# Kernel tuning notes

Hardware: AMD Instinct MI355X
Metric: run time of the kernel (lower is better)

The kernel has to match this reference:

```python
import jax, jax.numpy as jnp
import numpy as np

E, H = 1024, 16
HD = E // H
QLEN, KLEN, BS = 1024, 2048, 4
PREV = KLEN - QLEN


def _rel_shift(x):
    # x: (q, k, b, h) -> Transformer-XL relative shift
    q, k, b, h = x.shape
    x = jnp.pad(x, ((0, 0), (1, 0), (0, 0), (0, 0)))  # (q, k+1, b, h)
    x = x.reshape(k + 1, q, b, h)[1:].reshape(q, k, b, h)
    return x


def setup_inputs() -> dict:
    key = jax.random.key(0)
    ks = jax.random.split(key, 16)
    s = 0.02  # weight init scale
    inp = {
        "query": jax.random.normal(ks[0], (QLEN, BS, E), jnp.float32),
        "key": jax.random.normal(ks[1], (KLEN, BS, E), jnp.float32),
        "value": jax.random.normal(ks[2], (KLEN, BS, E), jnp.float32),
        "pos_embedding": jax.random.normal(ks[3], (KLEN, 1, E), jnp.float32),
        "U": jax.random.normal(ks[4], (H, HD), jnp.float32) * s,
        "V": jax.random.normal(ks[5], (H, HD), jnp.float32) * s,
        "Wq": jax.random.normal(ks[6], (E, E), jnp.float32) * s,
        "bq": jnp.zeros((E,), jnp.float32),
        "Wk": jax.random.normal(ks[7], (E, E), jnp.float32) * s,
        "bk": jnp.zeros((E,), jnp.float32),
        "Wv": jax.random.normal(ks[8], (E, E), jnp.float32) * s,
        "bv": jnp.zeros((E,), jnp.float32),
        "Wp": jax.random.normal(ks[9], (E, E), jnp.float32) * s,
        "Wo": jax.random.normal(ks[10], (E, E), jnp.float32) * s,
        "bo": jnp.zeros((E,), jnp.float32),
    }
    # causal XL mask: query i attends to keys j <= i + PREV; True = masked
    qi = jnp.arange(QLEN)[:, None]
    kj = jnp.arange(KLEN)[None, :]
    inp["mask"] = (kj > qi + PREV)[:, :, None]  # (q, k, 1) bool
    return inp


def reference(query, key, value, pos_embedding, U, V, Wq, bq, Wk, bk, Wv, bv, Wp, Wo, bo, mask):
    q_len, b, e = query.shape
    k_len = key.shape[0]
    scale = float(np.sqrt(e))  # note: sqrt(embed_dim), as in the source

    queries = (query @ Wq + bq).reshape(q_len, b, H, HD)
    keys = (key @ Wk + bk).reshape(k_len, b, H, HD)
    values = (value @ Wv + bv).reshape(k_len, b, H, HD)
    R = (pos_embedding @ Wp).reshape(-1, H, HD)  # (k, H, HD)

    content_score = jnp.einsum('qbhd,kbhd->qkbh', queries + U, keys)
    position_score = jnp.einsum('qbhd,khd->qkbh', queries + V, R)
    position_score = _rel_shift(position_score)

    attention_score = (content_score + position_score) / scale
    attention_score = jnp.where(mask[..., None], jnp.float32(-1e20), attention_score)
    attention = jax.nn.softmax(attention_score, axis=1)

    alpha = jnp.einsum('qkbh,kbhd->qbhd', attention, values).reshape(q_len, b, e)
    return alpha @ Wo + bo
```

## Files before the change

kernel.cpp:

```cpp
#include <hip/hip_runtime.h>
#include <stdint.h>

#define QLEN 1024
#define KLEN 2048
#define BSZ  4
#define NH   16
#define HD   64
#define EMB  1024
#define PREVL 1024
#define SLOG2E 0.045084220027780106f

typedef __attribute__((ext_vector_type(4))) float f32x4;
typedef __attribute__((ext_vector_type(8))) short bf16x8;

__device__ __forceinline__ unsigned short f2bf(float f){
  unsigned u = __float_as_uint(f);
  u += 0x7fffu + ((u >> 16) & 1u);
  return (unsigned short)(u >> 16);
}

__device__ __forceinline__ void gload_lds16(const void* g, void* l){
  __builtin_amdgcn_global_load_lds((const __attribute__((address_space(1))) void*)g,
                                   (__attribute__((address_space(3))) void*)l, 16, 0, 0);
}

__global__ void txl_prep(const float* __restrict__ w0, const float* __restrict__ w1,
                         const float* __restrict__ w2, const float* __restrict__ w3,
                         const float* __restrict__ w4,
                         unsigned short* __restrict__ o0, unsigned short* __restrict__ o1,
                         unsigned short* __restrict__ o2, unsigned short* __restrict__ o3,
                         unsigned short* __restrict__ o4,
                         const float* __restrict__ q, const float* __restrict__ k,
                         const float* __restrict__ v, const float* __restrict__ p,
                         unsigned short* __restrict__ qo, unsigned short* __restrict__ ko,
                         unsigned short* __restrict__ vo, unsigned short* __restrict__ po){
  const int bid = blockIdx.x;
  if (bid < 5120){
    const int z = bid >> 10, rem = bid & 1023;
    const int by = rem >> 5, bx = rem & 31;
    const float* in; unsigned short* out;
    switch (z){
      case 0: in = w0; out = o0; break;
      case 1: in = w1; out = o1; break;
      case 2: in = w2; out = o2; break;
      case 3: in = w3; out = o3; break;
      default: in = w4; out = o4; break;
    }
    __shared__ float tile[32][33];
    int tx = threadIdx.x & 31, ty = threadIdx.x >> 5;
    int k0 = by * 32, n0 = bx * 32;
    #pragma unroll
    for (int j = 0; j < 32; j += 8)
      tile[ty + j][tx] = in[(size_t)(k0 + ty + j) * EMB + n0 + tx];
    __syncthreads();
    #pragma unroll
    for (int j = 0; j < 32; j += 8)
      out[(size_t)(n0 + ty + j) * EMB + k0 + tx] = f2bf(tile[tx][ty + j]);
  } else {
    for (size_t c = (size_t)(bid - 5120) * 256 + threadIdx.x; c < 2883584; c += (size_t)2048 * 256){
      const float* src; unsigned short* dst; size_t off;
      if (c < 524288)      { src = q; dst = qo; off = c; }
      else if (c < 1572864){ src = k; dst = ko; off = c - 524288; }
      else if (c < 2621440){ src = v; dst = vo; off = c - 1572864; }
      else                 { src = p; dst = po; off = c - 2621440; }
      f32x4 a = *(const f32x4*)(src + off * 8);
      f32x4 b = *(const f32x4*)(src + off * 8 + 4);
      bf16x8 r;
      #pragma unroll
      for (int u = 0; u < 4; ++u){ r[u] = (short)f2bf(a[u]); r[u + 4] = (short)f2bf(b[u]); }
      *(bf16x8*)(dst + off * 8) = r;
    }
  }
}

__global__ __launch_bounds__(256)
void txl_gemm_proj(const unsigned short* __restrict__ pbf, const unsigned short* __restrict__ qbf,
                   const unsigned short* __restrict__ kbf, const unsigned short* __restrict__ vbf,
                   const unsigned short* __restrict__ WpT, const unsigned short* __restrict__ WqT,
                   const unsigned short* __restrict__ WkT, const unsigned short* __restrict__ WvT,
                   const float* __restrict__ bq, const float* __restrict__ bk,
                   const float* __restrict__ bv, const float* __restrict__ U,
                   const float* __restrict__ V,
                   unsigned short* __restrict__ Rb, unsigned short* __restrict__ Qu,
                   unsigned short* __restrict__ Qv, unsigned short* __restrict__ Kb,
                   unsigned short* __restrict__ Vt){
  const int bid = blockIdx.x;
  int mode, local;
  const unsigned short *Ag, *Wt;
  if (bid < 128)      { mode = 3; local = bid;       Ag = pbf; Wt = WpT; }
  else if (bid < 384) { mode = 0; local = bid - 128; Ag = qbf; Wt = WqT; }
  else if (bid < 896) { mode = 1; local = bid - 384; Ag = kbf; Wt = WkT; }
  else                { mode = 2; local = bid - 896; Ag = vbf; Wt = WvT; }
  const int m0 = (local >> 3) * 128, n0 = (local & 7) * 128;

  const int tid = threadIdx.x;
  const int lane = tid & 63, wave = tid >> 6;
  const int lr = lane & 15, lg = lane >> 4;
  const int wm = wave >> 1, wn = wave & 1;
  __shared__ unsigned short At[128 * 64];
  __shared__ unsigned short Bt[128 * 64];
  f32x4 acc[4][4] = {};

  for (int kt = 0; kt < EMB / 64; ++kt){
    const int k0 = kt * 64;
    __syncthreads();
    #pragma unroll
    for (int j = 0; j < 4; ++j){
      int row = j * 32 + (tid >> 3);
      int g = (tid & 7) ^ (row & 7);
      gload_lds16(Ag + (size_t)(m0 + row) * EMB + k0 + g * 8, &At[j * 2048 + wave * 512]);
      gload_lds16(Wt + (size_t)(n0 + row) * EMB + k0 + g * 8, &Bt[j * 2048 + wave * 512]);
    }
    __syncthreads();
    #pragma unroll
    for (int ks = 0; ks < 2; ++ks){
      bf16x8 af[4], bfr[4];
      #pragma unroll
      for (int mb = 0; mb < 4; ++mb){
        int row = wm * 64 + mb * 16 + lr;
        af[mb] = *(const bf16x8*)&At[row * 64 + ((lg + 4 * ks) ^ (row & 7)) * 8];
      }
      #pragma unroll
      for (int nb = 0; nb < 4; ++nb){
        int row = wn * 64 + nb * 16 + lr;
        bfr[nb] = *(const bf16x8*)&Bt[row * 64 + ((lg + 4 * ks) ^ (row & 7)) * 8];
      }
      __builtin_amdgcn_s_setprio(1);
      #pragma unroll
      for (int mb = 0; mb < 4; ++mb)
        #pragma unroll
        for (int nb = 0; nb < 4; ++nb)
          acc[mb][nb] = __builtin_amdgcn_mfma_f32_16x16x32_bf16(af[mb], bfr[nb], acc[mb][nb], 0, 0, 0);
      __builtin_amdgcn_s_setprio(0);
    }
  }
  #pragma unroll
  for (int mb = 0; mb < 4; ++mb){
    #pragma unroll
    for (int nb = 0; nb < 4; ++nb){
      #pragma unroll
      for (int i = 0; i < 4; ++i){
        int m = m0 + wm * 64 + mb * 16 + 4 * lg + i;
        int n = n0 + wn * 64 + nb * 16 + lr;
        float v = acc[mb][nb][i];
        if (mode == 0){
          int qq = m >> 2, b = m & 3, h = n >> 6, d = n & 63;
          size_t idx = ((((size_t)b * NH + h) * QLEN) + qq) * HD + d;
          float base = v + bq[n];
          Qu[idx] = f2bf((base + U[n]) * SLOG2E);
          Qv[idx] = f2bf((base + V[n]) * SLOG2E);
        } else if (mode == 1){
          int kp = m >> 2, b = m & 3, h = n >> 6, d = n & 63;
          Kb[((((size_t)b * NH + h) * KLEN) + kp) * HD + d] = f2bf(v + bk[n]);
        } else if (mode == 2){
          int kp = m >> 2, b = m & 3, h = n >> 6, d = n & 63;
          Vt[((((size_t)b * NH + h) * HD) + d) * KLEN + kp] = f2bf(v + bv[n]);
        } else {
          int h = n >> 6, d = n & 63;
          Rb[((size_t)h * KLEN + m) * HD + d] = f2bf(v);
        }
      }
    }
  }
}

__global__ __launch_bounds__(256)
void txl_gemm_out(const unsigned short* __restrict__ Ag, const unsigned short* __restrict__ Wt,
                  const float* __restrict__ bias, float* __restrict__ out0){
  const int tid = threadIdx.x;
  const int lane = tid & 63, wave = tid >> 6;
  const int lr = lane & 15, lg = lane >> 4;
  const int wm = wave >> 1, wn = wave & 1;
  const int m0 = blockIdx.y * 128, n0 = blockIdx.x * 128;
  __shared__ unsigned short At[128 * 64];
  __shared__ unsigned short Bt[128 * 64];
  f32x4 acc[4][4] = {};

  for (int kt = 0; kt < EMB / 64; ++kt){
    const int k0 = kt * 64;
    __syncthreads();
    #pragma unroll
    for (int j = 0; j < 4; ++j){
      int row = j * 32 + (tid >> 3);
      int g = (tid & 7) ^ (row & 7);
      gload_lds16(Ag + (size_t)(m0 + row) * EMB + k0 + g * 8, &At[j * 2048 + wave * 512]);
      gload_lds16(Wt + (size_t)(n0 + row) * EMB + k0 + g * 8, &Bt[j * 2048 + wave * 512]);
    }
    __syncthreads();
    #pragma unroll
    for (int ks = 0; ks < 2; ++ks){
      bf16x8 af[4], bfr[4];
      #pragma unroll
      for (int mb = 0; mb < 4; ++mb){
        int row = wm * 64 + mb * 16 + lr;
        af[mb] = *(const bf16x8*)&At[row * 64 + ((lg + 4 * ks) ^ (row & 7)) * 8];
      }
      #pragma unroll
      for (int nb = 0; nb < 4; ++nb){
        int row = wn * 64 + nb * 16 + lr;
        bfr[nb] = *(const bf16x8*)&Bt[row * 64 + ((lg + 4 * ks) ^ (row & 7)) * 8];
      }
      __builtin_amdgcn_s_setprio(1);
      #pragma unroll
      for (int mb = 0; mb < 4; ++mb)
        #pragma unroll
        for (int nb = 0; nb < 4; ++nb)
          acc[mb][nb] = __builtin_amdgcn_mfma_f32_16x16x32_bf16(af[mb], bfr[nb], acc[mb][nb], 0, 0, 0);
      __builtin_amdgcn_s_setprio(0);
    }
  }
  #pragma unroll
  for (int mb = 0; mb < 4; ++mb)
    #pragma unroll
    for (int nb = 0; nb < 4; ++nb)
      #pragma unroll
      for (int i = 0; i < 4; ++i){
        int m = m0 + wm * 64 + mb * 16 + 4 * lg + i;
        int n = n0 + wn * 64 + nb * 16 + lr;
        out0[(size_t)m * EMB + n] = acc[mb][nb][i] + bias[n];
      }
}

__global__ __launch_bounds__(256)
void txl_attn(const unsigned short* __restrict__ Qu, const unsigned short* __restrict__ Qv,
              const unsigned short* __restrict__ Kb, const unsigned short* __restrict__ Vt,
              const unsigned short* __restrict__ Rb, unsigned short* __restrict__ alpha){
  const int tid = threadIdx.x, lane = tid & 63, wave = tid >> 6;
  const int lr = lane & 15, lg = lane >> 4;
  const int qt = blockIdx.x, h = blockIdx.y, b = blockIdx.z;
  const int q0 = qt * 64;
  const int myq0 = q0 + 16 * wave;

  __shared__ union { unsigned short q[2][64 * 64]; unsigned short p[4][16 * 64]; } smq;
  __shared__ unsigned short sm_k[64 * 64];
  __shared__ unsigned short sm_v[64 * 64];
  __shared__ unsigned short sm_r[128 * 64];
  __shared__ float sm_t[4][16 * 81];

  const unsigned short* quB = Qu + (((size_t)b * NH + h) * QLEN) * HD;
  const unsigned short* qvB = Qv + (((size_t)b * NH + h) * QLEN) * HD;
  const unsigned short* kB  = Kb + (((size_t)b * NH + h) * KLEN) * HD;
  const unsigned short* vB  = Vt + (((size_t)b * NH + h) * HD) * KLEN;
  const unsigned short* rB  = Rb + ((size_t)h * KLEN) * HD;

  #pragma unroll
  for (int j = 0; j < 2; ++j){
    int row = j * 32 + (tid >> 3);
    int g = (tid & 7) ^ (row & 7);
    gload_lds16(quB + (size_t)(q0 + row) * HD + g * 8, &smq.q[0][j * 2048 + wave * 512]);
    gload_lds16(qvB + (size_t)(q0 + row) * HD + g * 8, &smq.q[1][j * 2048 + wave * 512]);
  }
  __syncthreads();
  bf16x8 qfu[2], qfv[2];
  {
    int row = 16 * wave + lr;
    #pragma unroll
    for (int ks = 0; ks < 2; ++ks){
      qfu[ks] = *(const bf16x8*)&smq.q[0][row * 64 + ((lg + 4 * ks) ^ (row & 7)) * 8];
      qfv[ks] = *(const bf16x8*)&smq.q[1][row * 64 + ((lg + 4 * ks) ^ (row & 7)) * 8];
    }
  }

  f32x4 o[4] = {};
  float ls[4] = {0.f, 0.f, 0.f, 0.f};

  const int nk0 = qt + 17;
  const int nk = nk0 < 32 ? nk0 : 32;
  const int roff = 48 - 16 * wave;

  for (int kt = 0; kt < nk; ++kt){
    const int k0 = kt * 64;
    const int rbase = k0 + (QLEN - 64) - q0;
    __syncthreads();
    #pragma unroll
    for (int j = 0; j < 2; ++j){
      int row = j * 32 + (tid >> 3);
      int g = (tid & 7) ^ (row & 7);
      gload_lds16(kB + (size_t)(k0 + row) * HD + g * 8, &sm_k[j * 2048 + wave * 512]);
      gload_lds16(vB + (size_t)row * KLEN + k0 + g * 8, &sm_v[j * 2048 + wave * 512]);
    }
    #pragma unroll
    for (int j = 0; j < 4; ++j){
      int row = j * 32 + (tid >> 3);
      int g = (tid & 7) ^ (row & 7);
      int r = rbase + row; if (r > KLEN - 1) r = KLEN - 1;
      gload_lds16(rB + (size_t)r * HD + g * 8, &sm_r[j * 2048 + wave * 512]);
    }
    __syncthreads();

    f32x4 sc[4] = {};
    f32x4 tt[5] = {};
    __builtin_amdgcn_s_setprio(1);
    #pragma unroll
    for (int ks = 0; ks < 2; ++ks){
      #pragma unroll
      for (int nb = 0; nb < 4; ++nb){
        int row = nb * 16 + lr;
        bf16x8 kf = *(const bf16x8*)&sm_k[row * 64 + ((lg + 4 * ks) ^ (row & 7)) * 8];
        sc[nb] = __builtin_amdgcn_mfma_f32_16x16x32_bf16(qfu[ks], kf, sc[nb], 0, 0, 0);
      }
      #pragma unroll
      for (int rb = 0; rb < 5; ++rb){
        int row = roff + rb * 16 + lr;
        bf16x8 rf = *(const bf16x8*)&sm_r[row * 64 + ((lg + 4 * ks) ^ (row & 7)) * 8];
        tt[rb] = __builtin_amdgcn_mfma_f32_16x16x32_bf16(qfv[ks], rf, tt[rb], 0, 0, 0);
      }
    }
    __builtin_amdgcn_s_setprio(0);

    float* tw = sm_t[wave];
    #pragma unroll
    for (int rb = 0; rb < 5; ++rb)
      #pragma unroll
      for (int i = 0; i < 4; ++i)
        tw[(4 * lg + i) * 81 + rb * 16 + lr] = tt[rb][i];
    asm volatile("s_waitcnt lgkmcnt(0)" ::: "memory");

    #pragma unroll
    for (int i = 0; i < 4; ++i){
      int qq = 4 * lg + i;
      int qglob = myq0 + qq;
      float rs = 0.f;
      #pragma unroll
      for (int nb = 0; nb < 4; ++nb){
        int kk = nb * 16 + lr;
        float tv = tw[qq * 81 + kk + 15 - qq];
        float s = sc[nb][i] + tv;
        if (k0 + kk > qglob + PREVL) s = -1e30f;
        float p = exp2f(s);
        rs += p;
        smq.p[wave][qq * 64 + (((kk >> 3) ^ (qq & 7)) << 3) + (kk & 7)] = f2bf(p);
      }
      ls[i] += rs;
    }
    asm volatile("s_waitcnt lgkmcnt(0)" ::: "memory");

    __builtin_amdgcn_s_setprio(1);
    #pragma unroll
    for (int ks = 0; ks < 2; ++ks){
      bf16x8 pa = *(const bf16x8*)&smq.p[wave][lr * 64 + ((lg + 4 * ks) ^ (lr & 7)) * 8];
      #pragma unroll
      for (int db = 0; db < 4; ++db){
        int row = db * 16 + lr;
        bf16x8 vf = *(const bf16x8*)&sm_v[row * 64 + ((lg + 4 * ks) ^ (row & 7)) * 8];
        o[db] = __builtin_amdgcn_mfma_f32_16x16x32_bf16(pa, vf, o[db], 0, 0, 0);
      }
    }
    __builtin_amdgcn_s_setprio(0);
  }

  #pragma unroll
  for (int i = 0; i < 4; ++i){
    float s = ls[i];
    s += __shfl_xor(s, 1); s += __shfl_xor(s, 2);
    s += __shfl_xor(s, 4); s += __shfl_xor(s, 8);
    float inv = 1.0f / s;
    int q = myq0 + 4 * lg + i;
    #pragma unroll
    for (int db = 0; db < 4; ++db){
      int e = (h << 6) + db * 16 + lr;
      alpha[((size_t)q * BSZ + b) * EMB + e] = f2bf(o[db][i] * inv);
    }
  }
}

extern "C" void kernel_launch(void* const* d_in, const int* in_sizes, int n_in,
                              void* d_out, int out_size, void* d_ws, size_t ws_size,
                              hipStream_t stream) {
  const float* query = (const float*)d_in[0];
  const float* key   = (const float*)d_in[1];
  const float* value = (const float*)d_in[2];
  const float* pos   = (const float*)d_in[3];
  const float* U     = (const float*)d_in[4];
  const float* V     = (const float*)d_in[5];
  const float* Wq    = (const float*)d_in[6];
  const float* bq    = (const float*)d_in[7];
  const float* Wk    = (const float*)d_in[8];
  const float* bk    = (const float*)d_in[9];
  const float* Wv    = (const float*)d_in[10];
  const float* bv    = (const float*)d_in[11];
  const float* Wp    = (const float*)d_in[12];
  const float* Wo    = (const float*)d_in[13];
  const float* bo    = (const float*)d_in[14];

  char* w = (char*)d_ws;
  const size_t MB = 1u << 20;
  unsigned short* WqT = (unsigned short*)(w + 0 * MB);
  unsigned short* WkT = (unsigned short*)(w + 2 * MB);
  unsigned short* WvT = (unsigned short*)(w + 4 * MB);
  unsigned short* WpT = (unsigned short*)(w + 6 * MB);
  unsigned short* WoT = (unsigned short*)(w + 8 * MB);
  unsigned short* Qu  = (unsigned short*)(w + 10 * MB);
  unsigned short* Qv  = (unsigned short*)(w + 18 * MB);
  unsigned short* Kb  = (unsigned short*)(w + 26 * MB);
  unsigned short* Vt  = (unsigned short*)(w + 42 * MB);
  unsigned short* Rb  = (unsigned short*)(w + 58 * MB);
  unsigned short* qbf = (unsigned short*)(w + 62 * MB);
  unsigned short* kbf = (unsigned short*)(w + 70 * MB);
  unsigned short* vbf = (unsigned short*)(w + 86 * MB);
  unsigned short* pbf = (unsigned short*)(w + 102 * MB);
  unsigned short* alpha = qbf;

  txl_prep<<<dim3(7168), 256, 0, stream>>>(Wq, Wk, Wv, Wp, Wo, WqT, WkT, WvT, WpT, WoT,
                                           query, key, value, pos, qbf, kbf, vbf, pbf);

  txl_gemm_proj<<<dim3(1408), 256, 0, stream>>>(pbf, qbf, kbf, vbf, WpT, WqT, WkT, WvT,
                                                bq, bk, bv, U, V, Rb, Qu, Qv, Kb, Vt);

  txl_attn<<<dim3(16, 16, 4), 256, 0, stream>>>(Qu, Qv, Kb, Vt, Rb, alpha);

  txl_gemm_out<<<dim3(8, 32), 256, 0, stream>>>(alpha, WoT, bo, (float*)d_out);
}
```

Measured before the change: 284.5 us.

## Shrink attention LDS: store positional scores as bf16 and load Q fragments directly

```diff
diff --git a/kernel.cpp b/kernel.cpp
--- a/kernel.cpp
+++ b/kernel.cpp
@@ -9,6 +9,7 @@
 #define EMB  1024
 #define PREVL 1024
 #define SLOG2E 0.045084220027780106f
+#define TPAD 83
 
 typedef __attribute__((ext_vector_type(4))) float f32x4;
 typedef __attribute__((ext_vector_type(8))) short bf16x8;
@@ -17,6 +18,12 @@
   unsigned u = __float_as_uint(f);
   u += 0x7fffu + ((u >> 16) & 1u);
   return (unsigned short)(u >> 16);
+}
+__device__ __forceinline__ unsigned short f2bf_trunc(float f){
+  return (unsigned short)(__float_as_uint(f) >> 16);
+}
+__device__ __forceinline__ float bf2f(unsigned short s){
+  return __uint_as_float(((unsigned)s) << 16);
 }
 
 __device__ __forceinline__ void gload_lds16(const void* g, void* l){
@@ -231,11 +238,11 @@
   const int q0 = qt * 64;
   const int myq0 = q0 + 16 * wave;
 
-  __shared__ union { unsigned short q[2][64 * 64]; unsigned short p[4][16 * 64]; } smq;
+  __shared__ unsigned short sm_p[4][16 * 64];
   __shared__ unsigned short sm_k[64 * 64];
   __shared__ unsigned short sm_v[64 * 64];
   __shared__ unsigned short sm_r[128 * 64];
-  __shared__ float sm_t[4][16 * 81];
+  __shared__ unsigned short sm_t[4][16 * TPAD];
 
   const unsigned short* quB = Qu + (((size_t)b * NH + h) * QLEN) * HD;
   const unsigned short* qvB = Qv + (((size_t)b * NH + h) * QLEN) * HD;
@@ -243,21 +250,13 @@
   const unsigned short* vB  = Vt + (((size_t)b * NH + h) * HD) * KLEN;
   const unsigned short* rB  = Rb + ((size_t)h * KLEN) * HD;
 
-  #pragma unroll
-  for (int j = 0; j < 2; ++j){
-    int row = j * 32 + (tid >> 3);
-    int g = (tid & 7) ^ (row & 7);
-    gload_lds16(quB + (size_t)(q0 + row) * HD + g * 8, &smq.q[0][j * 2048 + wave * 512]);
-    gload_lds16(qvB + (size_t)(q0 + row) * HD + g * 8, &smq.q[1][j * 2048 + wave * 512]);
-  }
-  __syncthreads();
   bf16x8 qfu[2], qfv[2];
   {
-    int row = 16 * wave + lr;
+    int qrow = myq0 + lr;
     #pragma unroll
     for (int ks = 0; ks < 2; ++ks){
-      qfu[ks] = *(const bf16x8*)&smq.q[0][row * 64 + ((lg + 4 * ks) ^ (row & 7)) * 8];
-      qfv[ks] = *(const bf16x8*)&smq.q[1][row * 64 + ((lg + 4 * ks) ^ (row & 7)) * 8];
+      qfu[ks] = *(const bf16x8*)(quB + (size_t)qrow * HD + (lg + 4 * ks) * 8);
+      qfv[ks] = *(const bf16x8*)(qvB + (size_t)qrow * HD + (lg + 4 * ks) * 8);
     }
   }
 
@@ -308,12 +307,12 @@
     }
     __builtin_amdgcn_s_setprio(0);
 
-    float* tw = sm_t[wave];
+    unsigned short* tw = sm_t[wave];
     #pragma unroll
     for (int rb = 0; rb < 5; ++rb)
       #pragma unroll
       for (int i = 0; i < 4; ++i)
-        tw[(4 * lg + i) * 81 + rb * 16 + lr] = tt[rb][i];
+        tw[(4 * lg + i) * TPAD + rb * 16 + lr] = f2bf_trunc(tt[rb][i]);
     asm volatile("s_waitcnt lgkmcnt(0)" ::: "memory");
 
     #pragma unroll
@@ -324,12 +323,12 @@
       #pragma unroll
       for (int nb = 0; nb < 4; ++nb){
         int kk = nb * 16 + lr;
-        float tv = tw[qq * 81 + kk + 15 - qq];
+        float tv = bf2f(tw[qq * TPAD + kk + 15 - qq]);
         float s = sc[nb][i] + tv;
         if (k0 + kk > qglob + PREVL) s = -1e30f;
         float p = exp2f(s);
         rs += p;
-        smq.p[wave][qq * 64 + (((kk >> 3) ^ (qq & 7)) << 3) + (kk & 7)] = f2bf(p);
+        sm_p[wave][qq * 64 + (((kk >> 3) ^ (qq & 7)) << 3) + (kk & 7)] = f2bf(p);
       }
       ls[i] += rs;
     }
@@ -338,7 +337,7 @@
     __builtin_amdgcn_s_setprio(1);
     #pragma unroll
     for (int ks = 0; ks < 2; ++ks){
-      bf16x8 pa = *(const bf16x8*)&smq.p[wave][lr * 64 + ((lg + 4 * ks) ^ (lr & 7)) * 8];
+      bf16x8 pa = *(const bf16x8*)&sm_p[wave][lr * 64 + ((lg + 4 * ks) ^ (lr & 7)) * 8];
       #pragma unroll
       for (int db = 0; db < 4; ++db){
         int row = db * 16 + lr;
```

Result: slower. 293.4 us (+3.1%).
